# Kernel optimization log

Hardware: AMD Instinct MI355X
Metric: run time of the kernel (lower is better)

The kernel has to match this reference:

```python
import jax, jax.numpy as jnp
import numpy as np

EPS = 1e-5


def _selective_scan(u, delta, A, Bm, Cm, D, delta_bias):
    # u, delta: (B, KD, L); A: (KD, N); Bm, Cm: (B, K, N, L); D, delta_bias: (KD,)
    Bb, KD, L = u.shape
    K = Bm.shape[1]
    Din = KD // K
    N = A.shape[1]
    delta = jax.nn.softplus(delta + delta_bias[None, :, None])            # (B,KD,L)
    dA = jnp.exp(delta[..., None] * A[None, :, None, :])                  # (B,KD,L,N)
    Bl = jnp.broadcast_to(Bm[:, :, None], (Bb, K, Din, N, L)).reshape(Bb, KD, N, L)
    Bl = jnp.moveaxis(Bl, -1, 2)                                          # (B,KD,L,N)
    dBu = (delta * u)[..., None] * Bl                                     # (B,KD,L,N)

    def comb(c1, c2):
        a1, b1 = c1
        a2, b2 = c2
        return a2 * a1, a2 * b1 + b2

    _, h = jax.lax.associative_scan(comb, (dA, dBu), axis=2)              # h: (B,KD,L,N)
    Cl = jnp.broadcast_to(Cm[:, :, None], (Bb, K, Din, N, L)).reshape(Bb, KD, N, L)
    Cl = jnp.moveaxis(Cl, -1, 2)
    y = jnp.sum(h * Cl, axis=-1) + D[None, :, None] * u                   # (B,KD,L)
    return y


def setup_inputs() -> dict:
    key = jax.random.key(0)
    ks = jax.random.split(key, 12)
    B, H, W, Dd = 1, 16, 16, 16
    C = 48            # d_model
    Din = 48          # d_inner (expand=1)
    N = 16            # d_state
    R = 3             # dt_rank = ceil(48/16)
    K = 8             # scan directions
    x = jax.random.normal(ks[0], (B, H, W, Dd, C), jnp.float32)
    in_proj_w = jax.random.normal(ks[1], (2 * Din, C), jnp.float32) * (C ** -0.5)
    conv_w = jax.random.normal(ks[2], (Din, 1, 3, 3, 3), jnp.float32) * 0.1
    conv_b = jax.random.normal(ks[3], (Din,), jnp.float32) * 0.01
    x_proj_weight = jax.random.normal(ks[4], (K, R + 2 * N, Din), jnp.float32) * (Din ** -0.5)
    dt_projs_weight = jax.random.uniform(ks[5], (K, Din, R), jnp.float32, -(R ** -0.5), R ** -0.5)
    # faithful dt bias init: inverse softplus of dt ~ logU(1e-3, 1e-1)
    u = jax.random.uniform(ks[6], (K, Din), jnp.float32)
    dt = jnp.exp(u * (np.log(0.1) - np.log(0.001)) + np.log(0.001))
    dt = jnp.clip(dt, 1e-4, None)
    dt_projs_bias = dt + jnp.log(-jnp.expm1(-dt))
    A_logs = jnp.log(jnp.broadcast_to(jnp.arange(1, N + 1, dtype=jnp.float32), (K * Din, N))).copy()
    Ds = jnp.ones((K * Din,), jnp.float32)
    norm_w = jnp.ones((Din,), jnp.float32)
    norm_b = jnp.zeros((Din,), jnp.float32)
    out_proj_w = jax.random.normal(ks[7], (C, Din), jnp.float32) * (Din ** -0.5)
    return {"x": x, "in_proj_w": in_proj_w, "conv_w": conv_w, "conv_b": conv_b,
            "x_proj_weight": x_proj_weight, "dt_projs_weight": dt_projs_weight,
            "dt_projs_bias": dt_projs_bias, "A_logs": A_logs, "Ds": Ds,
            "norm_w": norm_w, "norm_b": norm_b, "out_proj_w": out_proj_w}


def reference(x, in_proj_w, conv_w, conv_b, x_proj_weight, dt_projs_weight,
              dt_projs_bias, A_logs, Ds, norm_w, norm_b, out_proj_w):
    Bb, H, W, Dd, C = x.shape
    Din = in_proj_w.shape[0] // 2
    K = x_proj_weight.shape[0]
    R = dt_projs_weight.shape[2]
    N = A_logs.shape[1]
    L = H * W * Dd
    # in_proj and gate split
    xz = jnp.einsum('bhwdc,ec->bhwde', x, in_proj_w)
    xm, z = jnp.split(xz, 2, axis=-1)
    # depthwise 3D conv + SiLU (channels-first)
    xc = jnp.transpose(xm, (0, 4, 1, 2, 3))                               # (B,Din,H,W,D)
    xc = jax.lax.conv_general_dilated(xc, conv_w, (1, 1, 1), 'SAME',
                                      dimension_numbers=('NCDHW', 'OIDHW', 'NCDHW'),
                                      feature_group_count=Din)
    xc = jax.nn.silu(xc + conv_b[None, :, None, None, None])
    # 8 scan orderings: 4 axis permutations + their reversals
    x0 = xc.reshape(Bb, Din, L)
    x1 = jnp.transpose(xc, (0, 1, 3, 2, 4)).reshape(Bb, Din, L)
    x2 = jnp.transpose(xc, (0, 1, 4, 3, 2)).reshape(Bb, Din, L)
    x3 = jnp.transpose(xc, (0, 1, 2, 4, 3)).reshape(Bb, Din, L)
    x4s = jnp.stack([x0, x1, x2, x3], axis=1)                             # (B,4,Din,L)
    xs = jnp.concatenate([x4s, jnp.flip(x4s, axis=-1)], axis=1)           # (B,8,Din,L)
    # per-direction projections
    x_dbl = jnp.einsum('bkdl,kcd->bkcl', xs, x_proj_weight)
    dts, Bs, Cs = jnp.split(x_dbl, [R, R + N], axis=2)                    # (B,K,R,L),(B,K,N,L),(B,K,N,L)
    dts = jnp.einsum('bkrl,kdr->bkdl', dts, dt_projs_weight)              # (B,K,Din,L)
    u = xs.reshape(Bb, K * Din, L)
    delta = dts.reshape(Bb, K * Din, L)
    A = -jnp.exp(A_logs)                                                  # (K*Din, N)
    y = _selective_scan(u, delta, A, Bs, Cs, Ds, dt_projs_bias.reshape(-1))
    y = y.reshape(Bb, K, Din, L)
    # undo reversals and permutations, sum all directions
    yk = y[:, :4] + jnp.flip(y[:, 4:], axis=-1)                           # (B,4,Din,L)
    y0 = yk[:, 0].reshape(Bb, Din, H, W, Dd)
    y1 = jnp.transpose(yk[:, 1].reshape(Bb, Din, W, H, Dd), (0, 1, 3, 2, 4))
    y2 = jnp.transpose(yk[:, 2].reshape(Bb, Din, Dd, W, H), (0, 1, 4, 3, 2))
    y3 = jnp.transpose(yk[:, 3].reshape(Bb, Din, H, Dd, W), (0, 1, 2, 4, 3))
    ysum = y0 + y1 + y2 + y3                                              # (B,Din,H,W,D)
    # LayerNorm over channels, gate, out_proj
    yl = jnp.transpose(ysum, (0, 2, 3, 4, 1))                             # (B,H,W,D,Din)
    mu = jnp.mean(yl, axis=-1, keepdims=True)
    var = jnp.mean((yl - mu) ** 2, axis=-1, keepdims=True)
    yn = (yl - mu) * jax.lax.rsqrt(var + EPS) * norm_w + norm_b
    out = yn * jax.nn.silu(z)
    return jnp.einsum('bhwde,ce->bhwdc', out, out_proj_w)
```

## Files before the change

kernel.cpp:

```cpp
#include <hip/hip_runtime.h>
#include <hip/hip_bf16.h>
#include <math.h>

#define HH 16
#define WW 16
#define DD 16
#define LL 4096
#define CC 48
#define DIN 48
#define NN 16
#define RR 3
#define KK 8
#define KD 384
#define SNCH 64
#define SCHL 64

__global__ __launch_bounds__(256) void k_inproj(const float* __restrict__ x,
                                                const float* __restrict__ W,
                                                float* __restrict__ xm,
                                                float* __restrict__ z) {
    int tid = blockIdx.x * 256 + threadIdx.x;
    if (tid >= LL * 96) return;
    int e = tid % 96, l = tid / 96;
    const float4* xr = (const float4*)(x + l * CC);
    const float4* wr = (const float4*)(W + e * CC);
    float acc = 0.f;
#pragma unroll
    for (int c4 = 0; c4 < CC / 4; ++c4) {
        float4 a = xr[c4], b = wr[c4];
        acc += a.x * b.x + a.y * b.y + a.z * b.z + a.w * b.w;
    }
    if (e < DIN) xm[e * LL + l] = acc;
    else         z[l * DIN + (e - DIN)] = acc;
}

__global__ __launch_bounds__(256) void k_convscat(const float* __restrict__ xm,
                                                  const float* __restrict__ cw,
                                                  const float* __restrict__ cb,
                                                  float* __restrict__ xs) {
    int tid = blockIdx.x * 256 + threadIdx.x;
    if (tid >= DIN * LL) return;
    int s = tid & (LL - 1), d = tid >> 12;
    int dd = s & 15, w = (s >> 4) & 15, h = s >> 8;
    const float* wp = cw + d * 27;
    const float* xp = xm + d * LL;
    float acc = 0.f;
#pragma unroll
    for (int i = -1; i <= 1; ++i) {
        int hh = h + i; if (hh < 0 || hh > 15) continue;
#pragma unroll
        for (int j = -1; j <= 1; ++j) {
            int ww2 = w + j; if (ww2 < 0 || ww2 > 15) continue;
#pragma unroll
            for (int q = -1; q <= 1; ++q) {
                int dd2 = dd + q; if (dd2 < 0 || dd2 > 15) continue;
                acc += wp[(i + 1) * 9 + (j + 1) * 3 + (q + 1)]
                     * xp[hh * 256 + ww2 * 16 + dd2];
            }
        }
    }
    acc += cb[d];
    float v = acc / (1.f + __expf(-acc));
    int p0 = s;
    int p1 = w * 256 + h * 16 + dd;
    int p2 = dd * 256 + w * 16 + h;
    int p3 = h * 256 + dd * 16 + w;
    xs[(size_t)(0 * DIN + d) * LL + p0] = v;
    xs[(size_t)(1 * DIN + d) * LL + p1] = v;
    xs[(size_t)(2 * DIN + d) * LL + p2] = v;
    xs[(size_t)(3 * DIN + d) * LL + p3] = v;
    xs[(size_t)(4 * DIN + d) * LL + (LL - 1 - p0)] = v;
    xs[(size_t)(5 * DIN + d) * LL + (LL - 1 - p1)] = v;
    xs[(size_t)(6 * DIN + d) * LL + (LL - 1 - p2)] = v;
    xs[(size_t)(7 * DIN + d) * LL + (LL - 1 - p3)] = v;
}

__global__ __launch_bounds__(256) void k_xproj2(const float* __restrict__ xs,
                                                const float* __restrict__ xpw,
                                                const float* __restrict__ dtw,
                                                const float* __restrict__ dtb,
                                                float* __restrict__ BC,
                                                float* __restrict__ dsp) {
    int k = blockIdx.x >> 6;
    int l0 = (blockIdx.x & 63) * 64;
    int tid = threadIdx.x;
    __shared__ float xd[35 * 65];
    __shared__ float wl[35 * 49];
    for (int i = tid; i < 35 * 48; i += 256)
        wl[(i / 48) * 49 + (i % 48)] = xpw[k * 35 * 48 + i];
    __syncthreads();
#pragma unroll
    for (int it = 0; it < 3; ++it) {
        int item = it * 256 + tid;
        if (item < 560) {
            int c = item % 35, l4 = item / 35;
            const float4* xr = (const float4*)(xs + (size_t)k * DIN * LL + l0) + l4;
            const float* wr = wl + c * 49;
            float4 acc = {0.f, 0.f, 0.f, 0.f};
#pragma unroll
            for (int d2 = 0; d2 < 48; ++d2) {
                float4 v = xr[(size_t)d2 * (LL / 4)];
                float w = wr[d2];
                acc.x += v.x * w; acc.y += v.y * w; acc.z += v.z * w; acc.w += v.w * w;
            }
            float* o = xd + c * 65 + l4 * 4;
            o[0] = acc.x; o[1] = acc.y; o[2] = acc.z; o[3] = acc.w;
        }
    }
    __syncthreads();
#pragma unroll
    for (int it = 0; it < 8; ++it) {
        int idx = it * 256 + tid;
        int l = idx >> 5, c = idx & 31;
        BC[((size_t)k * LL + l0 + l) * 32 + c] = xd[(c + 3) * 65 + l];
    }
#pragma unroll
    for (int it = 0; it < 12; ++it) {
        int idx = it * 256 + tid;
        int d2 = idx >> 6, l = idx & 63;
        int gd = k * DIN + d2;
        float v = xd[l] * dtw[gd * 3] + xd[65 + l] * dtw[gd * 3 + 1]
                + xd[130 + l] * dtw[gd * 3 + 2] + dtb[gd];
        dsp[(size_t)gd * LL + l0 + l] = (v > 20.f) ? v : log1pf(__expf(v));
    }
}

__global__ __launch_bounds__(1024) void k_scanf(const float* __restrict__ xs,
                                                const float* __restrict__ dsp,
                                                const float* __restrict__ BC,
                                                const float* __restrict__ A_logs,
                                                const float* __restrict__ Ds,
                                                float* __restrict__ y2) {
    int gid = blockIdx.x;
    int k = gid / DIN;
    int d = gid - k * DIN;
    int t = threadIdx.x;
    int n = t & 15, c = t >> 4;
    __shared__ float u_lds[LL];
    __shared__ float d_lds[LL];
    __shared__ float pa_lds[SNCH * 16];
    __shared__ float hf_lds[SNCH * 16];
    __shared__ float h0_lds[SNCH * 16];
    {
        const float4* up4 = (const float4*)(xs + (size_t)gid * LL);
        const float4* dp4 = (const float4*)(dsp + (size_t)gid * LL);
        float4* ul = (float4*)u_lds;
        float4* dl = (float4*)d_lds;
        for (int i = t; i < LL / 4; i += 1024) { ul[i] = up4[i]; dl[i] = dp4[i]; }
    }
    __syncthreads();
    float A = -__expf(A_logs[gid * NN + n]);
    const float* bp = BC + ((size_t)k * LL + c * SCHL) * 32 + n;
    const float* cp = bp + 16;
    int base = c * SCHL;
    float h = 0.f, pa = 1.f;
#pragma unroll 4
    for (int i = 0; i < SCHL; ++i) {
        float delta = d_lds[base + i];
        float u = u_lds[base + i];
        float Bv = bp[(size_t)i * 32];
        float dA = __expf(delta * A);
        h = h * dA + delta * u * Bv;
        pa *= dA;
    }
    pa_lds[t] = pa;
    hf_lds[t] = h;
    __syncthreads();
    if (t < 16) {
        float hh = 0.f;
#pragma unroll 8
        for (int cc = 0; cc < SNCH; ++cc) {
            int idx = cc * 16 + t;
            h0_lds[idx] = hh;
            hh = hh * pa_lds[idx] + hf_lds[idx];
        }
    }
    __syncthreads();
    h = h0_lds[t];
    float Dv = Ds[gid];
#pragma unroll 4
    for (int i = 0; i < SCHL; ++i) {
        float delta = d_lds[base + i];
        float u = u_lds[base + i];
        float Bv = bp[(size_t)i * 32];
        float Cv = cp[(size_t)i * 32];
        float dA = __expf(delta * A);
        h = h * dA + delta * u * Bv;
        float p = h * Cv;
        p += __shfl_xor(p, 1, 64);
        p += __shfl_xor(p, 2, 64);
        p += __shfl_xor(p, 4, 64);
        p += __shfl_xor(p, 8, 64);
        if (n == 0) {
            int l = base + i;
            int ll = (k & 4) ? (LL - 1 - l) : l;
            int a = ll >> 8, b2 = (ll >> 4) & 15, c2 = ll & 15;
            int s;
            switch (k & 3) {
                case 0: s = ll;                        break;
                case 1: s = b2 * 256 + a * 16 + c2;    break;
                case 2: s = c2 * 256 + b2 * 16 + a;    break;
                default: s = a * 256 + c2 * 16 + b2;   break;
            }
            y2[((size_t)s * KK + k) * DIN + d] = p + Dv * u;
        }
    }
}

__global__ __launch_bounds__(256) void k_final2(const float* __restrict__ y2,
                                                const float* __restrict__ z,
                                                const float* __restrict__ nw,
                                                const float* __restrict__ nb,
                                                const float* __restrict__ opw,
                                                float* __restrict__ out) {
    int wv = threadIdx.x >> 6, lane = threadIdx.x & 63;
    int s = blockIdx.x * 4 + wv;
    __shared__ float g[4][DIN];
    float val = 0.f;
    if (lane < DIN) {
        const float* yp = y2 + (size_t)s * (KK * DIN) + lane;
#pragma unroll
        for (int k = 0; k < KK; ++k) val += yp[k * DIN];
    }
    float m = val;
#pragma unroll
    for (int o = 32; o >= 1; o >>= 1) m += __shfl_xor(m, o, 64);
    m *= (1.f / 48.f);
    float dv = (lane < DIN) ? (val - m) : 0.f;
    float v2 = dv * dv;
#pragma unroll
    for (int o = 32; o >= 1; o >>= 1) v2 += __shfl_xor(v2, o, 64);
    v2 *= (1.f / 48.f);
    float inv = rsqrtf(v2 + 1e-5f);
    if (lane < DIN) {
        float yn = dv * inv * nw[lane] + nb[lane];
        float zz = z[s * DIN + lane];
        g[wv][lane] = yn * (zz / (1.f + __expf(-zz)));
    }
    __syncthreads();
    if (lane < DIN) {
        const float* wr = opw + lane * DIN;
        float acc = 0.f;
#pragma unroll
        for (int e = 0; e < DIN; ++e) acc += g[wv][e] * wr[e];
        out[s * CC + lane] = acc;
    }
}

extern "C" void kernel_launch(void* const* d_in, const int* in_sizes, int n_in,
                              void* d_out, int out_size, void* d_ws, size_t ws_size,
                              hipStream_t stream) {
    const float* x      = (const float*)d_in[0];
    const float* ipw    = (const float*)d_in[1];
    const float* cw     = (const float*)d_in[2];
    const float* cb     = (const float*)d_in[3];
    const float* xpw    = (const float*)d_in[4];
    const float* dtw    = (const float*)d_in[5];
    const float* dtb    = (const float*)d_in[6];
    const float* A_logs = (const float*)d_in[7];
    const float* Ds     = (const float*)d_in[8];
    const float* nw     = (const float*)d_in[9];
    const float* nb     = (const float*)d_in[10];
    const float* opw    = (const float*)d_in[11];
    float* out = (float*)d_out;

    float* ws  = (float*)d_ws;
    float* xm  = ws;
    float* z   = xm + DIN * LL;
    float* xs  = z + LL * DIN;
    float* BC  = xs + (size_t)KD * LL;
    float* dsp = BC + (size_t)KK * LL * 32;
    float* y2  = dsp + (size_t)KD * LL;

    k_inproj<<<(LL * 96 + 255) / 256, 256, 0, stream>>>(x, ipw, xm, z);
    k_convscat<<<(DIN * LL + 255) / 256, 256, 0, stream>>>(xm, cw, cb, xs);
    k_xproj2<<<KK * 64, 256, 0, stream>>>(xs, xpw, dtw, dtb, BC, dsp);
    k_scanf<<<KD, 1024, 0, stream>>>(xs, dsp, BC, A_logs, Ds, y2);
    k_final2<<<LL / 4, 256, 0, stream>>>(y2, z, nw, nb, opw, out);
}
```

Before: 167.3 us.

## Stage scan output in LDS, add transpose kernel, and tile xs in xproj

The scan kernel now writes its outputs to padded shared memory and stores them contiguously per channel, instead of issuing scattered 4-byte stores to the permuted (s,k,d) layout. A new transpose kernel goes through shared memory to reorder those results into the layout the final kernel reads, using float4 stores. The scan's u/delta LDS arrays are padded per chunk to cut bank conflicts. The xproj kernel now loads its 48x64 xs tile into LDS once instead of reading it repeatedly from global memory. The cost is an extra kernel launch plus one more write and read of a 384x4096 intermediate.

Measured after the change: 174.5 us. 4.2% more time.

```diff
diff --git a/kernel.cpp b/kernel.cpp
--- a/kernel.cpp
+++ b/kernel.cpp
@@ -14,6 +14,7 @@
 #define KD 384
 #define SNCH 64
 #define SCHL 64
+#define PCH 68
 
 __global__ __launch_bounds__(256) void k_inproj(const float* __restrict__ x,
                                                 const float* __restrict__ W,
@@ -84,22 +85,29 @@
     int k = blockIdx.x >> 6;
     int l0 = (blockIdx.x & 63) * 64;
     int tid = threadIdx.x;
+    __shared__ float xt[48 * 68];
     __shared__ float xd[35 * 65];
     __shared__ float wl[35 * 49];
     for (int i = tid; i < 35 * 48; i += 256)
         wl[(i / 48) * 49 + (i % 48)] = xpw[k * 35 * 48 + i];
+#pragma unroll
+    for (int it = 0; it < 3; ++it) {
+        int idx = it * 256 + tid;
+        int d = idx >> 4, w = idx & 15;
+        float4 v = ((const float4*)(xs + (size_t)(k * DIN + d) * LL + l0))[w];
+        ((float4*)(xt + d * 68))[w] = v;
+    }
     __syncthreads();
 #pragma unroll
     for (int it = 0; it < 3; ++it) {
         int item = it * 256 + tid;
         if (item < 560) {
             int c = item % 35, l4 = item / 35;
-            const float4* xr = (const float4*)(xs + (size_t)k * DIN * LL + l0) + l4;
             const float* wr = wl + c * 49;
             float4 acc = {0.f, 0.f, 0.f, 0.f};
 #pragma unroll
             for (int d2 = 0; d2 < 48; ++d2) {
-                float4 v = xr[(size_t)d2 * (LL / 4)];
+                float4 v = ((const float4*)(xt + d2 * 68))[l4];
                 float w = wr[d2];
                 acc.x += v.x * w; acc.y += v.y * w; acc.z += v.z * w; acc.w += v.w * w;
             }
@@ -130,29 +138,29 @@
                                                 const float* __restrict__ BC,
                                                 const float* __restrict__ A_logs,
                                                 const float* __restrict__ Ds,
-                                                float* __restrict__ y2) {
+                                                float* __restrict__ y4) {
     int gid = blockIdx.x;
     int k = gid / DIN;
-    int d = gid - k * DIN;
     int t = threadIdx.x;
     int n = t & 15, c = t >> 4;
-    __shared__ float u_lds[LL];
-    __shared__ float d_lds[LL];
+    __shared__ float u_lds[SNCH * PCH];
+    __shared__ float d_lds[SNCH * PCH];
+    __shared__ float y_lds[SNCH * PCH];
     __shared__ float pa_lds[SNCH * 16];
     __shared__ float hf_lds[SNCH * 16];
     __shared__ float h0_lds[SNCH * 16];
     {
-        const float4* up4 = (const float4*)(xs + (size_t)gid * LL);
-        const float4* dp4 = (const float4*)(dsp + (size_t)gid * LL);
-        float4* ul = (float4*)u_lds;
-        float4* dl = (float4*)d_lds;
-        for (int i = t; i < LL / 4; i += 1024) { ul[i] = up4[i]; dl[i] = dp4[i]; }
+        int c2 = t >> 4, w = t & 15;
+        float4 uv = ((const float4*)(xs + (size_t)gid * LL))[t];
+        float4 dv = ((const float4*)(dsp + (size_t)gid * LL))[t];
+        ((float4*)u_lds)[c2 * (PCH / 4) + w] = uv;
+        ((float4*)d_lds)[c2 * (PCH / 4) + w] = dv;
     }
     __syncthreads();
     float A = -__expf(A_logs[gid * NN + n]);
     const float* bp = BC + ((size_t)k * LL + c * SCHL) * 32 + n;
     const float* cp = bp + 16;
-    int base = c * SCHL;
+    int base = c * PCH;
     float h = 0.f, pa = 1.f;
 #pragma unroll 4
     for (int i = 0; i < SCHL; ++i) {
@@ -191,19 +199,49 @@
         p += __shfl_xor(p, 2, 64);
         p += __shfl_xor(p, 4, 64);
         p += __shfl_xor(p, 8, 64);
-        if (n == 0) {
-            int l = base + i;
-            int ll = (k & 4) ? (LL - 1 - l) : l;
-            int a = ll >> 8, b2 = (ll >> 4) & 15, c2 = ll & 15;
-            int s;
-            switch (k & 3) {
-                case 0: s = ll;                        break;
-                case 1: s = b2 * 256 + a * 16 + c2;    break;
-                case 2: s = c2 * 256 + b2 * 16 + a;    break;
-                default: s = a * 256 + c2 * 16 + b2;   break;
-            }
-            y2[((size_t)s * KK + k) * DIN + d] = p + Dv * u;
+        if (n == 0) y_lds[base + i] = p + Dv * u;
+    }
+    __syncthreads();
+    {
+        int c2 = t >> 4, w = t & 15;
+        float4 v = ((const float4*)y_lds)[c2 * (PCH / 4) + w];
+        ((float4*)(y4 + (size_t)gid * LL))[t] = v;
+    }
+}
+
+__global__ __launch_bounds__(256) void k_trans(const float* __restrict__ y4,
+                                               float* __restrict__ y2) {
+    int k = blockIdx.x >> 5;
+    int l0 = (blockIdx.x & 31) * 128;
+    int tid = threadIdx.x;
+    __shared__ float ty[48 * 129];
+#pragma unroll
+    for (int it = 0; it < 24; ++it) {
+        int idx = it * 256 + tid;
+        int l = idx & 127, d = idx >> 7;
+        ty[d * 129 + l] = y4[(size_t)(k * DIN + d) * LL + l0 + l];
+    }
+    __syncthreads();
+#pragma unroll
+    for (int it = 0; it < 6; ++it) {
+        int idx = it * 256 + tid;
+        int l = idx / 12, g = idx % 12;
+        int lg = l0 + l;
+        int ll = (k & 4) ? (LL - 1 - lg) : lg;
+        int a = ll >> 8, b2 = (ll >> 4) & 15, c2 = ll & 15;
+        int s;
+        switch (k & 3) {
+            case 0: s = ll;                        break;
+            case 1: s = b2 * 256 + a * 16 + c2;    break;
+            case 2: s = c2 * 256 + b2 * 16 + a;    break;
+            default: s = a * 256 + c2 * 16 + b2;   break;
         }
+        float4 v;
+        v.x = ty[(g * 4 + 0) * 129 + l];
+        v.y = ty[(g * 4 + 1) * 129 + l];
+        v.z = ty[(g * 4 + 2) * 129 + l];
+        v.w = ty[(g * 4 + 3) * 129 + l];
+        ((float4*)(y2 + (size_t)s * KD))[k * 12 + g] = v;
     }
 }
 
@@ -270,11 +308,13 @@
     float* xs  = z + LL * DIN;
     float* BC  = xs + (size_t)KD * LL;
     float* dsp = BC + (size_t)KK * LL * 32;
-    float* y2  = dsp + (size_t)KD * LL;
+    float* y4  = dsp + (size_t)KD * LL;
+    float* y2  = y4 + (size_t)KD * LL;
 
     k_inproj<<<(LL * 96 + 255) / 256, 256, 0, stream>>>(x, ipw, xm, z);
     k_convscat<<<(DIN * LL + 255) / 256, 256, 0, stream>>>(xm, cw, cb, xs);
     k_xproj2<<<KK * 64, 256, 0, stream>>>(xs, xpw, dtw, dtb, BC, dsp);
-    k_scanf<<<KD, 1024, 0, stream>>>(xs, dsp, BC, A_logs, Ds, y2);
+    k_scanf<<<KD, 1024, 0, stream>>>(xs, dsp, BC, A_logs, Ds, y4);
+    k_trans<<<KK * 32, 256, 0, stream>>>(y4, y2);
     k_final2<<<LL / 4, 256, 0, stream>>>(y2, z, nw, nb, opw, out);
 }
```

## Fuse x_proj with scan pass one and split chunked scan into three kernels

Applied to the files above, without the earlier changes.

The x_proj/dt kernel now also runs the first chunk-local scan pass, reading B, delta and u straight from shared memory, and writes per-chunk decay products and end states to global memory. A small kernel combines the chunk carries, and a third kernel parallelised over (direction, chunk) reruns the chunk scan from its carry-in. The y output is staged in shared memory so it is written as coalesced float4 stores instead of scattered scalars. This removes the 384-block scan kernel with its full-sequence LDS loads and serial single-wave carry step, at the cost of two extra launches and extra global traffic for the chunk states.

New measurement: 167.9 us. Within noise of the previous version (+0.3%).

```diff
diff --git a/kernel.cpp b/kernel.cpp
--- a/kernel.cpp
+++ b/kernel.cpp
@@ -12,8 +12,8 @@
 #define RR 3
 #define KK 8
 #define KD 384
-#define SNCH 64
-#define SCHL 64
+#define NCH 64
+#define CHL 64
 
 __global__ __launch_bounds__(256) void k_inproj(const float* __restrict__ x,
                                                 const float* __restrict__ W,
@@ -75,113 +75,124 @@
     xs[(size_t)(7 * DIN + d) * LL + (LL - 1 - p3)] = v;
 }
 
-__global__ __launch_bounds__(256) void k_xproj2(const float* __restrict__ xs,
+__global__ __launch_bounds__(768) void k_xscan1(const float* __restrict__ xs,
                                                 const float* __restrict__ xpw,
                                                 const float* __restrict__ dtw,
                                                 const float* __restrict__ dtb,
+                                                const float* __restrict__ A_logs,
                                                 float* __restrict__ BC,
-                                                float* __restrict__ dsp) {
+                                                float* __restrict__ dsp,
+                                                float* __restrict__ pa_g,
+                                                float* __restrict__ hf_g) {
     int k = blockIdx.x >> 6;
-    int l0 = (blockIdx.x & 63) * 64;
+    int c = blockIdx.x & (NCH - 1);
+    int l0 = c * CHL;
     int tid = threadIdx.x;
+    __shared__ float xt[48 * 68];
     __shared__ float xd[35 * 65];
     __shared__ float wl[35 * 49];
-    for (int i = tid; i < 35 * 48; i += 256)
+    __shared__ float dt[48 * 68];
+    for (int i = tid; i < 35 * 48; i += 768)
         wl[(i / 48) * 49 + (i % 48)] = xpw[k * 35 * 48 + i];
-    __syncthreads();
-#pragma unroll
-    for (int it = 0; it < 3; ++it) {
-        int item = it * 256 + tid;
-        if (item < 560) {
-            int c = item % 35, l4 = item / 35;
-            const float4* xr = (const float4*)(xs + (size_t)k * DIN * LL + l0) + l4;
-            const float* wr = wl + c * 49;
-            float4 acc = {0.f, 0.f, 0.f, 0.f};
-#pragma unroll
-            for (int d2 = 0; d2 < 48; ++d2) {
-                float4 v = xr[(size_t)d2 * (LL / 4)];
-                float w = wr[d2];
-                acc.x += v.x * w; acc.y += v.y * w; acc.z += v.z * w; acc.w += v.w * w;
-            }
-            float* o = xd + c * 65 + l4 * 4;
-            o[0] = acc.x; o[1] = acc.y; o[2] = acc.z; o[3] = acc.w;
+    {
+        int d = tid >> 4, w = tid & 15;
+        float4 v = ((const float4*)(xs + (size_t)(k * DIN + d) * LL + l0))[w];
+        ((float4*)(xt + d * 68))[w] = v;
+    }
+    __syncthreads();
+    if (tid < 560) {
+        int cc = tid % 35, l4 = tid / 35;
+        const float* wr = wl + cc * 49;
+        float4 acc = {0.f, 0.f, 0.f, 0.f};
+#pragma unroll
+        for (int d2 = 0; d2 < 48; ++d2) {
+            float4 v = ((const float4*)(xt + d2 * 68))[l4];
+            float w = wr[d2];
+            acc.x += v.x * w; acc.y += v.y * w; acc.z += v.z * w; acc.w += v.w * w;
         }
-    }
-    __syncthreads();
-#pragma unroll
-    for (int it = 0; it < 8; ++it) {
-        int idx = it * 256 + tid;
-        int l = idx >> 5, c = idx & 31;
-        BC[((size_t)k * LL + l0 + l) * 32 + c] = xd[(c + 3) * 65 + l];
-    }
-#pragma unroll
-    for (int it = 0; it < 12; ++it) {
-        int idx = it * 256 + tid;
+        float* o = xd + cc * 65 + l4 * 4;
+        o[0] = acc.x; o[1] = acc.y; o[2] = acc.z; o[3] = acc.w;
+    }
+    __syncthreads();
+    if (tid < 512) {
+        int l = tid >> 3, q = tid & 7;
+        float4 v;
+#pragma unroll
+        for (int j = 0; j < 4; ++j) (&v.x)[j] = xd[(3 + q * 4 + j) * 65 + l];
+        ((float4*)(BC + ((size_t)(k * LL + l0 + l)) * 32))[q] = v;
+    }
+#pragma unroll
+    for (int r = 0; r < 4; ++r) {
+        int idx = r * 768 + tid;
         int d2 = idx >> 6, l = idx & 63;
         int gd = k * DIN + d2;
         float v = xd[l] * dtw[gd * 3] + xd[65 + l] * dtw[gd * 3 + 1]
                 + xd[130 + l] * dtw[gd * 3 + 2] + dtb[gd];
-        dsp[(size_t)gd * LL + l0 + l] = (v > 20.f) ? v : log1pf(__expf(v));
-    }
-}
-
-__global__ __launch_bounds__(1024) void k_scanf(const float* __restrict__ xs,
-                                                const float* __restrict__ dsp,
-                                                const float* __restrict__ BC,
-                                                const float* __restrict__ A_logs,
-                                                const float* __restrict__ Ds,
-                                                float* __restrict__ y2) {
-    int gid = blockIdx.x;
-    int k = gid / DIN;
-    int d = gid - k * DIN;
-    int t = threadIdx.x;
-    int n = t & 15, c = t >> 4;
-    __shared__ float u_lds[LL];
-    __shared__ float d_lds[LL];
-    __shared__ float pa_lds[SNCH * 16];
-    __shared__ float hf_lds[SNCH * 16];
-    __shared__ float h0_lds[SNCH * 16];
-    {
-        const float4* up4 = (const float4*)(xs + (size_t)gid * LL);
-        const float4* dp4 = (const float4*)(dsp + (size_t)gid * LL);
-        float4* ul = (float4*)u_lds;
-        float4* dl = (float4*)d_lds;
-        for (int i = t; i < LL / 4; i += 1024) { ul[i] = up4[i]; dl[i] = dp4[i]; }
-    }
-    __syncthreads();
+        float sp = (v > 20.f) ? v : log1pf(__expf(v));
+        dt[d2 * 68 + l] = sp;
+        dsp[(size_t)gd * LL + l0 + l] = sp;
+    }
+    __syncthreads();
+    int d = tid >> 4, n = tid & 15;
+    int gid = k * DIN + d;
     float A = -__expf(A_logs[gid * NN + n]);
-    const float* bp = BC + ((size_t)k * LL + c * SCHL) * 32 + n;
-    const float* cp = bp + 16;
-    int base = c * SCHL;
     float h = 0.f, pa = 1.f;
 #pragma unroll 4
-    for (int i = 0; i < SCHL; ++i) {
-        float delta = d_lds[base + i];
-        float u = u_lds[base + i];
-        float Bv = bp[(size_t)i * 32];
+    for (int i = 0; i < CHL; ++i) {
+        float delta = dt[d * 68 + i];
+        float u = xt[d * 68 + i];
+        float Bv = xd[(3 + n) * 65 + i];
         float dA = __expf(delta * A);
         h = h * dA + delta * u * Bv;
         pa *= dA;
     }
-    pa_lds[t] = pa;
-    hf_lds[t] = h;
-    __syncthreads();
-    if (t < 16) {
-        float hh = 0.f;
-#pragma unroll 8
-        for (int cc = 0; cc < SNCH; ++cc) {
-            int idx = cc * 16 + t;
-            h0_lds[idx] = hh;
-            hh = hh * pa_lds[idx] + hf_lds[idx];
-        }
-    }
-    __syncthreads();
-    h = h0_lds[t];
+    size_t si = (size_t)gid * (NCH * 16) + c * 16 + n;
+    pa_g[si] = pa;
+    hf_g[si] = h;
+}
+
+__global__ __launch_bounds__(256) void k_scan2(const float* __restrict__ pa_g,
+                                               const float* __restrict__ hf_g,
+                                               float* __restrict__ h0_g) {
+    int t = blockIdx.x * 256 + threadIdx.x;
+    if (t >= KD * NN) return;
+    int n = t & 15;
+    int gid = t >> 4;
+    size_t base = (size_t)gid * (NCH * 16) + n;
+    float h = 0.f;
+#pragma unroll 4
+    for (int c = 0; c < NCH; ++c) {
+        size_t idx = base + (size_t)c * 16;
+        h0_g[idx] = h;
+        h = h * pa_g[idx] + hf_g[idx];
+    }
+}
+
+__global__ __launch_bounds__(768) void k_scan3(const float* __restrict__ xs,
+                                               const float* __restrict__ dsp,
+                                               const float* __restrict__ BC,
+                                               const float* __restrict__ A_logs,
+                                               const float* __restrict__ Ds,
+                                               const float* __restrict__ h0_g,
+                                               float* __restrict__ y2) {
+    int k = blockIdx.x >> 6;
+    int c = blockIdx.x & (NCH - 1);
+    int l0 = c * CHL;
+    int tid = threadIdx.x;
+    int d = tid >> 4, n = tid & 15;
+    int gid = k * DIN + d;
+    __shared__ float y_t[48 * 68];
+    float A = -__expf(A_logs[gid * NN + n]);
     float Dv = Ds[gid];
+    float h = h0_g[(size_t)gid * (NCH * 16) + c * 16 + n];
+    const float* up = xs + (size_t)gid * LL + l0;
+    const float* dp = dsp + (size_t)gid * LL + l0;
+    const float* bp = BC + ((size_t)(k * LL + l0)) * 32 + n;
+    const float* cp = bp + 16;
 #pragma unroll 4
-    for (int i = 0; i < SCHL; ++i) {
-        float delta = d_lds[base + i];
-        float u = u_lds[base + i];
+    for (int i = 0; i < CHL; ++i) {
+        float delta = dp[i];
+        float u = up[i];
         float Bv = bp[(size_t)i * 32];
         float Cv = cp[(size_t)i * 32];
         float dA = __expf(delta * A);
@@ -191,19 +202,25 @@
         p += __shfl_xor(p, 2, 64);
         p += __shfl_xor(p, 4, 64);
         p += __shfl_xor(p, 8, 64);
-        if (n == 0) {
-            int l = base + i;
-            int ll = (k & 4) ? (LL - 1 - l) : l;
-            int a = ll >> 8, b2 = (ll >> 4) & 15, c2 = ll & 15;
-            int s;
-            switch (k & 3) {
-                case 0: s = ll;                        break;
-                case 1: s = b2 * 256 + a * 16 + c2;    break;
-                case 2: s = c2 * 256 + b2 * 16 + a;    break;
-                default: s = a * 256 + c2 * 16 + b2;   break;
-            }
-            y2[((size_t)s * KK + k) * DIN + d] = p + Dv * u;
+        if (n == 0) y_t[d * 68 + i] = p + Dv * u;
+    }
+    __syncthreads();
+    {
+        int g = tid >> 6, l = tid & 63;
+        int lg = l0 + l;
+        int ll = (k & 4) ? (LL - 1 - lg) : lg;
+        int a = ll >> 8, b2 = (ll >> 4) & 15, c2 = ll & 15;
+        int s;
+        switch (k & 3) {
+            case 0: s = ll;                        break;
+            case 1: s = b2 * 256 + a * 16 + c2;    break;
+            case 2: s = c2 * 256 + b2 * 16 + a;    break;
+            default: s = a * 256 + c2 * 16 + b2;   break;
         }
+        float4 v;
+#pragma unroll
+        for (int j = 0; j < 4; ++j) (&v.x)[j] = y_t[(g * 4 + j) * 68 + l];
+        ((float4*)(y2 + (size_t)s * KD + k * DIN))[g] = v;
     }
 }
 
@@ -218,7 +235,7 @@
     __shared__ float g[4][DIN];
     float val = 0.f;
     if (lane < DIN) {
-        const float* yp = y2 + (size_t)s * (KK * DIN) + lane;
+        const float* yp = y2 + (size_t)s * KD + lane;
 #pragma unroll
         for (int k = 0; k < KK; ++k) val += yp[k * DIN];
     }
@@ -264,17 +281,22 @@
     const float* opw    = (const float*)d_in[11];
     float* out = (float*)d_out;
 
-    float* ws  = (float*)d_ws;
-    float* xm  = ws;
-    float* z   = xm + DIN * LL;
-    float* xs  = z + LL * DIN;
-    float* BC  = xs + (size_t)KD * LL;
-    float* dsp = BC + (size_t)KK * LL * 32;
-    float* y2  = dsp + (size_t)KD * LL;
+    float* ws   = (float*)d_ws;
+    float* xm   = ws;
+    float* z    = xm + DIN * LL;
+    float* xs   = z + LL * DIN;
+    float* BC   = xs + (size_t)KD * LL;
+    float* dsp  = BC + (size_t)KK * LL * 32;
+    float* y2   = dsp + (size_t)KD * LL;
+    float* pa_g = y2 + (size_t)LL * KD;
+    float* hf_g = pa_g + (size_t)KD * NCH * 16;
+    float* h0_g = hf_g + (size_t)KD * NCH * 16;
 
     k_inproj<<<(LL * 96 + 255) / 256, 256, 0, stream>>>(x, ipw, xm, z);
     k_convscat<<<(DIN * LL + 255) / 256, 256, 0, stream>>>(xm, cw, cb, xs);
-    k_xproj2<<<KK * 64, 256, 0, stream>>>(xs, xpw, dtw, dtb, BC, dsp);
-    k_scanf<<<KD, 1024, 0, stream>>>(xs, dsp, BC, A_logs, Ds, y2);
+    k_xscan1<<<KK * NCH, 768, 0, stream>>>(xs, xpw, dtw, dtb, A_logs,
+                                           BC, dsp, pa_g, hf_g);
+    k_scan2<<<(KD * NN + 255) / 256, 256, 0, stream>>>(pa_g, hf_g, h0_g);
+    k_scan3<<<KK * NCH, 768, 0, stream>>>(xs, dsp, BC, A_logs, Ds, h0_g, y2);
     k_final2<<<LL / 4, 256, 0, stream>>>(y2, z, nw, nb, opw, out);
 }
```
